# Optimization experiments

Hardware: AMD Instinct MI355X
Metric: run time of the kernel (lower is better)

The kernel has to match this reference:

```python
import jax, jax.numpy as jnp
import numpy as np

B, L, D, H, DFF, MODES, ELAYERS = 64, 512, 512, 8, 2048, 32, 2
VOCAB, NUM_APP, KERNEL = 10000, 10000, 25
E = D // H


def setup_inputs() -> dict:
    key = jax.random.key(0)
    ks = jax.random.split(key, 16)
    scale = 1.0 / (D * D)  # FourierBlock weight init scale
    return {
        'x_app': jax.random.randint(ks[0], (B, L), 0, VOCAB),
        'x_time': jax.random.uniform(ks[1], (B, L), dtype=jnp.float32),
        'time_vecs': jax.random.normal(ks[2], (B, L, 24), dtype=jnp.float32),
        'targets': jax.random.randint(ks[3], (B,), 0, NUM_APP),
        'app_emb_w': jax.random.normal(ks[4], (VOCAB, D), dtype=jnp.float32) * 0.02,
        'time_w': jax.random.normal(ks[5], (D,), dtype=jnp.float32) * 0.02,
        'time_b': jnp.zeros((D,), jnp.float32),
        'Wq': jax.random.normal(ks[6], (ELAYERS, D, D), dtype=jnp.float32) * 0.02,
        'bq': jnp.zeros((ELAYERS, D), jnp.float32),
        'Wo': jax.random.normal(ks[7], (ELAYERS, D, D), dtype=jnp.float32) * 0.02,
        'bo': jnp.zeros((ELAYERS, D), jnp.float32),
        'four_wr': jax.random.uniform(ks[8], (ELAYERS, H, E, E, MODES), dtype=jnp.float32) * scale,
        'four_wi': jax.random.uniform(ks[9], (ELAYERS, H, E, E, MODES), dtype=jnp.float32) * scale,
        'conv1_w': jax.random.normal(ks[10], (ELAYERS, DFF, D), dtype=jnp.float32) * 0.02,
        'conv2_w': jax.random.normal(ks[11], (ELAYERS, D, DFF), dtype=jnp.float32) * 0.02,
        'norm_w': jnp.ones((D,), jnp.float32),
        'norm_b': jnp.zeros((D,), jnp.float32),
        'proj_w': jax.random.normal(ks[12], (NUM_APP, D + 24), dtype=jnp.float32) * 0.02,
        'proj_b': jnp.zeros((NUM_APP,), jnp.float32),
    }


def moving_avg(x):
    # edge-replicate pad by (K-1)//2 on each side, then AvgPool1d(K, stride=1)
    pad = (KERNEL - 1) // 2
    xp = jnp.pad(x, ((0, 0), (pad, pad), (0, 0)), mode='edge')  # [B, L+K-1, D]
    cs = jnp.cumsum(xp, axis=1)
    cs = jnp.concatenate([jnp.zeros_like(cs[:, :1]), cs], axis=1)
    return (cs[:, KERNEL:] - cs[:, :-KERNEL]) / KERNEL  # [B, L, D]


def series_decomp(x):
    m = moving_avg(x)
    return x - m, m


def my_layernorm(x, w, b, eps=1e-5):
    mu = jnp.mean(x, axis=-1, keepdims=True)
    var = jnp.mean((x - mu) ** 2, axis=-1, keepdims=True)
    xh = (x - mu) * jax.lax.rsqrt(var + eps) * w + b
    # my_Layernorm: subtract per-sample mean over the sequence dim
    return xh - jnp.mean(xh, axis=1, keepdims=True)


def fourier_block(q, wr, wi):
    # q: [B, L, H, E] -> [B, H, E, L]
    Bq, Lq, Hq, Eq = q.shape
    x = jnp.transpose(q, (0, 2, 3, 1))
    x_ft = jnp.fft.rfft(x, axis=-1)             # [B,H,E,L//2+1] complex64
    xs = x_ft[..., :MODES]                      # low-frequency mode selection
    w = (wr + 1j * wi).astype(xs.dtype)         # [H,E,E,M]
    out_sel = jnp.einsum('bhim,hiom->bhom', xs, w)
    out_ft = jnp.zeros((Bq, Hq, Eq, Lq // 2 + 1), dtype=xs.dtype).at[..., :MODES].set(out_sel)
    return jnp.fft.irfft(out_ft, n=Lq, axis=-1)  # [B,H,E,L]


def encoder_layer(x, Wq, bq, Wo, bo, wr, wi, c1, c2):
    Bx, Lx, Dx = x.shape
    q = (x @ Wq.T + bq).reshape(Bx, Lx, H, E)
    out = fourier_block(q, wr, wi)               # [B,H,E,L]
    # faithful to torch: out.view(B, L, -1) is a raw row-major reinterpret
    out = out.reshape(Bx, Lx, H * E)
    new_x = out @ Wo.T + bo
    x = x + new_x
    x, _ = series_decomp(x)
    y = jax.nn.relu(jnp.einsum('bld,fd->blf', x, c1))   # conv1 (1x1, no bias)
    y = jnp.einsum('blf,df->bld', y, c2)                # conv2 (1x1, no bias)
    res, _ = series_decomp(x + y)
    return res


def reference(x_app, x_time, time_vecs, targets, app_emb_w, time_w, time_b,
              Wq, bq, Wo, bo, four_wr, four_wi, conv1_w, conv2_w,
              norm_w, norm_b, proj_w, proj_b):
    x = app_emb_w[x_app] + x_time[..., None] * time_w + time_b  # [B,L,D]
    for l in range(ELAYERS):
        x = encoder_layer(x, Wq[l], bq[l], Wo[l], bo[l],
                          four_wr[l], four_wi[l], conv1_w[l], conv2_w[l])
    x = my_layernorm(x, norm_w, norm_b)
    last = x[:, -1, :]                                   # [B,D]
    out = jnp.concatenate([last, time_vecs[:, -1, :]], axis=1)  # [B,D+24]
    score = out @ proj_w.T + proj_b                      # [B,NUM_APP]
    return score  # mode='predict' returns score
```

## Files before the change

### kernel.cpp

```cpp
#include <hip/hip_runtime.h>


typedef unsigned short u16;
typedef float f32x4 __attribute__((ext_vector_type(4)));
typedef __bf16 bf16x8 __attribute__((ext_vector_type(8)));

__device__ __forceinline__ u16 f2b(float f) {
  unsigned u = __float_as_uint(f);
  return (u16)((u + 0x7FFFu + ((u >> 16) & 1u)) >> 16);
}
__device__ __forceinline__ float b2f(u16 v) {
  return __uint_as_float((unsigned)v << 16);
}
__device__ __forceinline__ f32x4 b4f(ushort4 v) {
  f32x4 r;
  r.x = b2f(v.x); r.y = b2f(v.y); r.z = b2f(v.z); r.w = b2f(v.w);
  return r;
}

__device__ __forceinline__ void gll16(const void* g, void* l) {
  __builtin_amdgcn_global_load_lds(
      (const __attribute__((address_space(1))) void*)g,
      (__attribute__((address_space(3))) void*)l, 16, 0, 0);
}

template<bool SWAP>
__device__ __forceinline__ f32x4 mfma16(bf16x8 a, bf16x8 b, f32x4 c) {
  if constexpr (SWAP)
    return __builtin_amdgcn_mfma_f32_16x16x32_bf16(b, a, c, 0, 0, 0);
  else
    return __builtin_amdgcn_mfma_f32_16x16x32_bf16(a, b, c, 0, 0, 0);
}

template<bool BIAS, bool RELU, bool RES, bool OUTBF16, bool GUARD, bool TRANS,
         bool SWZ>
__global__ __launch_bounds__(256, 3)
void k_gemm(const u16* __restrict__ A, const u16* __restrict__ B,
            const float* __restrict__ bias, const u16* __restrict__ res,
            float* __restrict__ Cf, u16* __restrict__ Cb,
            int M, int N, int K,
            long zA, long zB, long zC, int nbn, int nbm)
{
  __shared__ __align__(16) u16 sA[2][128 * 32];
  __shared__ __align__(16) u16 sB[2][128 * 32];
  const int tid = threadIdx.x;
  const int wave = tid >> 6, lane = tid & 63;
  int bn, bm;
  if (SWZ) {
    int bid = blockIdx.x;
    int xcd = bid & 7, loc = bid >> 3;
    bn = loc % nbn;
    bm = xcd * (nbm >> 3) + loc / nbn;
  } else {
    bn = blockIdx.x;
    bm = blockIdx.y;
  }
  const int bz = blockIdx.z;
  const int wm = (wave >> 1) * 64, wn = (wave & 1) * 64;

  A += (size_t)bz * zA;
  B += (size_t)bz * zB;

  const int r0 = tid >> 2;
  const int lg = tid & 3;
  const int ps = lg ^ ((r0 >> 1) & 3);
  int gmA0 = bm * 128 + r0, gmA1 = gmA0 + 64;
  int gnB0 = bn * 128 + r0, gnB1 = gnB0 + 64;
  if (GUARD) {
    gmA0 = gmA0 < M ? gmA0 : M - 1;
    gmA1 = gmA1 < M ? gmA1 : M - 1;
    gnB0 = gnB0 < N ? gnB0 : N - 1;
    gnB1 = gnB1 < N ? gnB1 : N - 1;
  }
  const size_t rb = (size_t)K * 2;
  const char* pa0 = (const char*)A + (size_t)gmA0 * rb + lg * 16;
  const char* pa1 = (const char*)A + (size_t)gmA1 * rb + lg * 16;
  const char* pb0 = (const char*)B + (size_t)gnB0 * rb + lg * 16;
  const char* pb1 = (const char*)B + (size_t)gnB1 * rb + lg * 16;
  const int w0 = r0 * 32 + ps * 8;

  f32x4 acc[4][4];
  const f32x4 z = {0.f, 0.f, 0.f, 0.f};
#pragma unroll
  for (int i = 0; i < 4; ++i)
#pragma unroll
    for (int j = 0; j < 4; ++j) acc[i][j] = z;

  const int r = lane & 15, qd = lane >> 4;
  const int pA = (qd ^ ((lane >> 1) & 3)) * 8;
  const int nk = K >> 5;

  uint4 va0, va1, vb0, vb1;
  auto gload = [&](int kt) {
    const size_t ko = (size_t)kt * 64;
    va0 = *(const uint4*)(pa0 + ko);
    va1 = *(const uint4*)(pa1 + ko);
    vb0 = *(const uint4*)(pb0 + ko);
    vb1 = *(const uint4*)(pb1 + ko);
  };

  gload(0);
  int pg = 0;
  for (int kt = 0; kt < nk; ++kt) {
    *(uint4*)&sA[pg][w0]        = va0;
    *(uint4*)&sA[pg][w0 + 2048] = va1;
    *(uint4*)&sB[pg][w0]        = vb0;
    *(uint4*)&sB[pg][w0 + 2048] = vb1;
    if (kt + 1 < nk) gload(kt + 1);
    __syncthreads();
    bf16x8 af[4], bg[4];
#pragma unroll
    for (int mi = 0; mi < 4; ++mi)
      af[mi] = *(const bf16x8*)&sA[pg][(wm + mi * 16 + r) * 32 + pA];
#pragma unroll
    for (int ni = 0; ni < 4; ++ni)
      bg[ni] = *(const bf16x8*)&sB[pg][(wn + ni * 16 + r) * 32 + pA];
#pragma unroll
    for (int mi = 0; mi < 4; ++mi)
#pragma unroll
      for (int ni = 0; ni < 4; ++ni)
        acc[mi][ni] = mfma16<!TRANS>(af[mi], bg[ni], acc[mi][ni]);
    pg ^= 1;
  }

  if (Cf) Cf += (size_t)bz * zC;
  if (Cb) Cb += (size_t)bz * zC;

  if constexpr (!TRANS) {
#pragma unroll
    for (int mi = 0; mi < 4; ++mi) {
      const int gm = bm * 128 + wm + mi * 16 + r;
      if (GUARD && gm >= M) continue;
#pragma unroll
      for (int ni = 0; ni < 4; ++ni) {
        const int gn0 = bn * 128 + wn + ni * 16 + qd * 4;
        if (GUARD && gn0 >= N) continue;
        float v[4];
        ushort4 rv;
        if (RES) rv = *(const ushort4*)&res[(size_t)gm * N + gn0];
#pragma unroll
        for (int e = 0; e < 4; ++e) {
          v[e] = acc[mi][ni][e];
          if (BIAS) v[e] += bias[gn0 + e];
          if (RES)  v[e] += b2f(e == 0 ? rv.x : e == 1 ? rv.y : e == 2 ? rv.z : rv.w);
          if (RELU) v[e] = v[e] > 0.f ? v[e] : 0.f;
        }
        if (OUTBF16) {
          ushort4 o;
          o.x = f2b(v[0]); o.y = f2b(v[1]); o.z = f2b(v[2]); o.w = f2b(v[3]);
          *(ushort4*)&Cb[(size_t)gm * N + gn0] = o;
        } else {
          float4 o = {v[0], v[1], v[2], v[3]};
          *(float4*)&Cf[(size_t)gm * N + gn0] = o;
        }
      }
    }
  } else {
#pragma unroll
    for (int ni = 0; ni < 4; ++ni) {
      const int gn = bn * 128 + wn + ni * 16 + r;
      if (GUARD && gn >= N) continue;
      const float bb = BIAS ? bias[gn] : 0.f;
#pragma unroll
      for (int mi = 0; mi < 4; ++mi) {
        const int gm0 = bm * 128 + wm + mi * 16 + qd * 4;
        if (GUARD && gm0 >= M) continue;
        float v[4];
#pragma unroll
        for (int e = 0; e < 4; ++e) {
          v[e] = acc[mi][ni][e];
          if (BIAS) v[e] += bb;
          if (RELU) v[e] = v[e] > 0.f ? v[e] : 0.f;
        }
        if (OUTBF16) {
          ushort4 o;
          o.x = f2b(v[0]); o.y = f2b(v[1]); o.z = f2b(v[2]); o.w = f2b(v[3]);
          *(ushort4*)&Cb[(size_t)gn * M + gm0] = o;
        } else {
          float4 o = {v[0], v[1], v[2], v[3]};
          *(float4*)&Cf[(size_t)gn * M + gm0] = o;
        }
      }
    }
  }
}

template<bool BIAS, bool RELU, bool RES, bool TRANS>
__global__ __launch_bounds__(512, 2)
void k_gemm3(const u16* __restrict__ A, const u16* __restrict__ B,
             const float* __restrict__ bias, const u16* __restrict__ res,
             u16* __restrict__ C, int M, int N, int K,
             int nbn, int nbm, long zA, long zC)
{
  __shared__ __align__(16) u16 sA[2][2][256 * 32];
  __shared__ __align__(16) u16 sB[2][2][256 * 32];
  const int tid = threadIdx.x;
  const int w8 = tid >> 6, lane = tid & 63;
  const int bid = blockIdx.x;
  const int xcd = bid & 7, loc = bid >> 3;
  const int mpx = (int)(gridDim.x >> 3) / nbn;
  const int mflat = xcd * mpx + loc / nbn;
  const int bn = loc % nbn;
  const int bz = mflat / nbm;
  const int bm = mflat - bz * nbm;
  const int wm = (w8 >> 2) * 128, wn = (w8 & 3) * 64;

  A += (size_t)bz * zA;

  const int r0 = tid >> 2;
  const int lg = (tid & 3) ^ ((r0 >> 1) & 3);
  const u16* pA0 = A + (size_t)(bm * 256 + r0) * K + lg * 8;
  const u16* pA1 = pA0 + (size_t)128 * K;
  const u16* pB0 = B + (size_t)(bn * 256 + r0) * K + lg * 8;
  const u16* pB1 = pB0 + (size_t)128 * K;
  const int la0 = w8 * 512;
  const int la1 = 4096 + w8 * 512;

  const int nk = K >> 6;

  auto stA = [&](int t, int ks) {
    const size_t ko = (size_t)(t << 6) + (size_t)(ks << 5);
    u16* d = &sA[t & 1][ks][0];
    gll16(pA0 + ko, d + la0);
    gll16(pA1 + ko, d + la1);
  };
  auto stB = [&](int t, int ks) {
    const size_t ko = (size_t)(t << 6) + (size_t)(ks << 5);
    u16* d = &sB[t & 1][ks][0];
    gll16(pB0 + ko, d + la0);
    gll16(pB1 + ko, d + la1);
  };

  f32x4 acc[8][4];
  const f32x4 z = {0.f, 0.f, 0.f, 0.f};
#pragma unroll
  for (int i = 0; i < 8; ++i)
#pragma unroll
    for (int j = 0; j < 4; ++j) acc[i][j] = z;

  const int fr = lane & 15, qd = lane >> 4;
  const int pAo = ((qd ^ ((lane >> 1) & 3)) << 3);

  stA(0, 0); stB(0, 0); stA(0, 1); stB(0, 1);
  if (nk > 1) { stA(1, 0); stB(1, 0); }
  asm volatile("s_waitcnt vmcnt(8)" ::: "memory");
  __builtin_amdgcn_s_barrier();

  for (int t = 0; t < nk; ++t) {
    const int c = t & 1;
    bf16x8 af[4], bgk[4];
#pragma unroll
    for (int i = 0; i < 4; ++i)
      af[i] = *(const bf16x8*)&sA[c][0][(wm + i * 16 + fr) * 32 + pAo];
#pragma unroll
    for (int i = 0; i < 4; ++i)
      bgk[i] = *(const bf16x8*)&sB[c][0][(wn + i * 16 + fr) * 32 + pAo];
    if (t + 1 < nk) stA(t + 1, 1);
    asm volatile("s_waitcnt vmcnt(8)" ::: "memory");
    __builtin_amdgcn_s_barrier();
    __builtin_amdgcn_s_setprio(1);
#pragma unroll
    for (int mi = 0; mi < 4; ++mi)
#pragma unroll
      for (int ni = 0; ni < 4; ++ni)
        acc[mi][ni] = __builtin_amdgcn_mfma_f32_16x16x32_bf16(
            af[mi], bgk[ni], acc[mi][ni], 0, 0, 0);
    __builtin_amdgcn_s_setprio(0);
    __builtin_amdgcn_s_barrier();
#pragma unroll
    for (int i = 0; i < 4; ++i)
      af[i] = *(const bf16x8*)&sA[c][0][(wm + 64 + i * 16 + fr) * 32 + pAo];
    if (t + 1 < nk) stB(t + 1, 1);
    if (t == nk - 1) asm volatile("s_waitcnt vmcnt(0)" ::: "memory");
    else             asm volatile("s_waitcnt vmcnt(8)" ::: "memory");
    __builtin_amdgcn_s_barrier();
    __builtin_amdgcn_s_setprio(1);
#pragma unroll
    for (int mi = 0; mi < 4; ++mi)
#pragma unroll
      for (int ni = 0; ni < 4; ++ni)
        acc[4 + mi][ni] = __builtin_amdgcn_mfma_f32_16x16x32_bf16(
            af[mi], bgk[ni], acc[4 + mi][ni], 0, 0, 0);
    __builtin_amdgcn_s_setprio(0);
    __builtin_amdgcn_s_barrier();
#pragma unroll
    for (int i = 0; i < 4; ++i)
      af[i] = *(const bf16x8*)&sA[c][1][(wm + i * 16 + fr) * 32 + pAo];
#pragma unroll
    for (int i = 0; i < 4; ++i)
      bgk[i] = *(const bf16x8*)&sB[c][1][(wn + i * 16 + fr) * 32 + pAo];
    if (t + 2 < nk) stA(t + 2, 0);
    asm volatile("s_waitcnt vmcnt(8)" ::: "memory");
    __builtin_amdgcn_s_barrier();
    __builtin_amdgcn_s_setprio(1);
#pragma unroll
    for (int mi = 0; mi < 4; ++mi)
#pragma unroll
      for (int ni = 0; ni < 4; ++ni)
        acc[mi][ni] = __builtin_amdgcn_mfma_f32_16x16x32_bf16(
            af[mi], bgk[ni], acc[mi][ni], 0, 0, 0);
    __builtin_amdgcn_s_setprio(0);
    __builtin_amdgcn_s_barrier();
#pragma unroll
    for (int i = 0; i < 4; ++i)
      af[i] = *(const bf16x8*)&sA[c][1][(wm + 64 + i * 16 + fr) * 32 + pAo];
    if (t + 2 < nk) stB(t + 2, 0);
    if (t == nk - 2) asm volatile("s_waitcnt vmcnt(4)" ::: "memory");
    else             asm volatile("s_waitcnt vmcnt(8)" ::: "memory");
    __builtin_amdgcn_s_barrier();
    __builtin_amdgcn_s_setprio(1);
#pragma unroll
    for (int mi = 0; mi < 4; ++mi)
#pragma unroll
      for (int ni = 0; ni < 4; ++ni)
        acc[4 + mi][ni] = __builtin_amdgcn_mfma_f32_16x16x32_bf16(
            af[mi], bgk[ni], acc[4 + mi][ni], 0, 0, 0);
    __builtin_amdgcn_s_setprio(0);
    __builtin_amdgcn_s_barrier();
  }

  C += (size_t)bz * zC;
#pragma unroll
  for (int mi = 0; mi < 8; ++mi) {
#pragma unroll
    for (int ni = 0; ni < 4; ++ni) {
#pragma unroll
      for (int e = 0; e < 4; ++e) {
        int gm = bm * 256 + wm + mi * 16 + qd * 4 + e;
        int gn = bn * 256 + wn + ni * 16 + fr;
        float v = acc[mi][ni][e];
        if (BIAS) v += bias[gn];
        if (RES)  v += b2f(res[(size_t)gm * N + gn]);
        if (RELU) v = v > 0.f ? v : 0.f;
        size_t oi = TRANS ? ((size_t)gn * M + gm) : ((size_t)gm * N + gn);
        C[oi] = f2b(v);
      }
    }
  }
}

__global__ void k_basis(u16* __restrict__ dftB, u16* __restrict__ Binv)
{
  int id = blockIdx.x * 256 + threadIdx.x;
  if (id >= 32768) return;
  {
    int m = id >> 9, l = id & 511;
    int mm = m & 31;
    float ang = (float)((l * mm) & 511) * (6.283185307179586f / 512.f);
    float s, c;
    __sincosf(ang, &s, &c);
    dftB[id] = f2b(m < 32 ? c : -s);
  }
  {
    int l = id >> 6, m = id & 63;
    int mm = m & 31;
    float ang = (float)((l * mm) & 511) * (6.283185307179586f / 512.f);
    float s, c;
    __sincosf(ang, &s, &c);
    float v;
    if (m < 32) v = (m == 0 ? 1.f : 2.f) * (1.f / 512.f) * c;
    else        v = (mm == 0 ? 0.f : (-2.f / 512.f) * s);
    Binv[id] = f2b(v);
  }
}

__global__ void k_convert4(const float* __restrict__ wq, u16* __restrict__ wqo,
                           const float* __restrict__ wo, u16* __restrict__ woo,
                           const float* __restrict__ c1, u16* __restrict__ c1o,
                           const float* __restrict__ c2, u16* __restrict__ c2o)
{
  int id = blockIdx.x * 256 + threadIdx.x;
  if (id < 524288)       wqo[id]           = f2b(wq[id]);
  else if (id < 1048576) woo[id - 524288]  = f2b(wo[id - 524288]);
  else if (id < 3145728) c1o[id - 1048576] = f2b(c1[id - 1048576]);
  else                   c2o[id - 3145728] = f2b(c2[id - 3145728]);
}

__global__ void k_convproj(const float* __restrict__ w, u16* __restrict__ o)
{
  int id = blockIdx.x * 256 + threadIdx.x;
  if (id >= 10000 * 544) return;
  int n = id / 544, k = id % 544;
  o[id] = f2b(k < 536 ? w[(size_t)n * 536 + k] : 0.f);
}

__global__ void k_transp(const float* __restrict__ wr, const float* __restrict__ wi,
                         float* __restrict__ wrT, float* __restrict__ wiT)
{
  __shared__ float tr[64 * 33], ti[64 * 33];
  int blk = blockIdx.x;
  int t = threadIdx.x;
  int lh = blk >> 6, i = blk & 63;
  const size_t src = (size_t)blk * 2048;
#pragma unroll
  for (int p = 0; p < 8; ++p) {
    int id = p * 256 + t;
    int o = id >> 5, m = id & 31;
    tr[o * 33 + m] = wr[src + id];
    ti[o * 33 + m] = wi[src + id];
  }
  __syncthreads();
#pragma unroll
  for (int p = 0; p < 8; ++p) {
    int id = p * 256 + t;
    int m = id >> 6, o = id & 63;
    size_t dst = ((size_t)(lh * 32 + m) * 64 + i) * 64 + o;
    wrT[dst] = tr[o * 33 + m];
    wiT[dst] = ti[o * 33 + m];
  }
}

__global__ void k_embed(const int* __restrict__ xapp, const float* __restrict__ xtime,
                        const float* __restrict__ emb, const float* __restrict__ tw,
                        const float* __restrict__ tb, u16* __restrict__ xb)
{
  int id = blockIdx.x * 256 + threadIdx.x;
  int j = id & 127, bl = id >> 7;
  float4 e = ((const float4*)emb)[(size_t)xapp[bl] * 128 + j];
  float t = xtime[bl];
  float4 w4 = ((const float4*)tw)[j];
  float4 b4 = ((const float4*)tb)[j];
  ushort4 o;
  o.x = f2b(e.x + t * w4.x + b4.x);
  o.y = f2b(e.y + t * w4.y + b4.y);
  o.z = f2b(e.z + t * w4.z + b4.z);
  o.w = f2b(e.w + t * w4.w + b4.w);
  ((ushort4*)xb)[id] = o;
}

__global__ __launch_bounds__(256)
void k_mix(const float* __restrict__ spec, const float* __restrict__ wrT,
           const float* __restrict__ wiT, u16* __restrict__ Ab)
{
  __shared__ float swr[4096], swi[4096];
  __shared__ float sre[4][64], sim[4][64];
  int hm = blockIdx.x;
  int bg = blockIdx.y;
  int h = hm >> 5, m = hm & 31, t = threadIdx.x;
  const float* wrb = wrT + (size_t)hm * 4096;
  const float* wib = wiT + (size_t)hm * 4096;
#pragma unroll
  for (int p = 0; p < 16; ++p) {
    int id = p * 256 + t;
    swr[id] = wrb[id];
    swi[id] = wib[id];
  }
  int o = t & 63, bsub = t >> 6;
  for (int b0 = 0; b0 < 16; b0 += 4) {
    __syncthreads();
    int b = bg * 16 + b0 + bsub;
    const float* spb = spec + (size_t)b * 32768;
    sre[bsub][o] = spb[m * 512 + h * 64 + o];
    sim[bsub][o] = spb[(32 + m) * 512 + h * 64 + o];
    __syncthreads();
    float aR = 0.f, aI = 0.f;
#pragma unroll 8
    for (int i = 0; i < 64; ++i) {
      float xr = sre[bsub][i], xi = sim[bsub][i];
      float wrv = swr[i * 64 + o], wiv = swi[i * 64 + o];
      aR += xr * wrv - xi * wiv;
      aI += xr * wiv + xi * wrv;
    }
    size_t row = (size_t)b * 512 + h * 64 + o;
    Ab[row * 64 + m] = f2b(aR);
    Ab[row * 64 + 32 + m] = f2b(aI);
  }
}

__global__ void k_decomp(const u16* __restrict__ in, u16* __restrict__ outb)
{
  int blk = blockIdx.x;
  int j = blk >> 3;
  int b = (blk & 7) + 8 * (j >> 3);
  int ck = (j & 7) * 2 + (threadIdx.x >> 7);
  int d4 = threadIdx.x & 127;
  const ushort4* xb = (const ushort4*)(in + (size_t)b * 262144) + d4;
  ushort4* ob = (ushort4*)(outb + (size_t)b * 262144) + d4;
  int l0 = ck * 32;
  f32x4 sum = {0.f, 0.f, 0.f, 0.f};
#pragma unroll
  for (int jj = -12; jj <= 12; ++jj) {
    int idx = l0 + jj;
    idx = idx < 0 ? 0 : idx;
    sum += b4f(xb[idx * 128]);
  }
#pragma unroll 4
  for (int l = l0; l < l0 + 32; ++l) {
    f32x4 xv = b4f(xb[l * 128]);
    f32x4 o = xv - sum * (1.f / 25.f);
    ushort4 ov;
    ov.x = f2b(o.x); ov.y = f2b(o.y); ov.z = f2b(o.z); ov.w = f2b(o.w);
    ob[l * 128] = ov;
    int ia = l + 13 > 511 ? 511 : l + 13;
    int ir = l - 12 < 0 ? 0 : l - 12;
    sum += b4f(xb[ia * 128]) - b4f(xb[ir * 128]);
  }
}

__global__ void k_lnstats(const u16* __restrict__ x, float* __restrict__ mu,
                          float* __restrict__ rs)
{
  int row = blockIdx.x;
  const u16* xr = x + (size_t)row * 512;
  int t = threadIdx.x;
  ushort2 p = ((const ushort2*)xr)[t];
  float v0 = b2f(p.x), v1 = b2f(p.y);
  float s = v0 + v1, ss = v0 * v0 + v1 * v1;
#pragma unroll
  for (int off = 32; off; off >>= 1) {
    s += __shfl_down(s, off);
    ss += __shfl_down(ss, off);
  }
  __shared__ float as[4], ass[4];
  if ((t & 63) == 0) { as[t >> 6] = s; ass[t >> 6] = ss; }
  __syncthreads();
  if (t == 0) {
    float S = as[0] + as[1] + as[2] + as[3];
    float SS = ass[0] + ass[1] + ass[2] + ass[3];
    float m = S * (1.f / 512.f);
    float var = SS * (1.f / 512.f) - m * m;
    mu[row] = m;
    rs[row] = rsqrtf(var + 1e-5f);
  }
}

__global__ void k_lastcat1(const u16* __restrict__ x, const float* __restrict__ mu,
                           const float* __restrict__ rs, float* __restrict__ part)
{
  int b = blockIdx.x >> 3, g = blockIdx.x & 7, t = threadIdx.x;
  const u16* xb = x + (size_t)b * 262144;
  const float* mub = mu + b * 512;
  const float* rsb = rs + b * 512;
  float a0 = 0.f, a1 = 0.f;
#pragma unroll 4
  for (int l = g * 64; l < g * 64 + 64; ++l) {
    float m = mub[l], rr = rsb[l];
    ushort2 p = ((const ushort2*)(xb + l * 512))[t];
    a0 += (b2f(p.x) - m) * rr;
    a1 += (b2f(p.y) - m) * rr;
  }
  part[((size_t)b * 8 + g) * 512 + 2 * t]     = a0;
  part[((size_t)b * 8 + g) * 512 + 2 * t + 1] = a1;
}

__global__ void k_lastcat2(const u16* __restrict__ x, const float* __restrict__ mu,
                           const float* __restrict__ rs, const float* __restrict__ part,
                           const float* __restrict__ nw, u16* __restrict__ cat)
{
  int b = blockIdx.x, t = threadIdx.x;
#pragma unroll
  for (int hh = 0; hh < 2; ++hh) {
    int d = t + hh * 256;
    float acc = 0.f;
#pragma unroll
    for (int g = 0; g < 8; ++g)
      acc += part[((size_t)b * 8 + g) * 512 + d];
    float lastv = (b2f(x[(size_t)b * 262144 + 511 * 512 + d]) - mu[b * 512 + 511])
                  * rs[b * 512 + 511];
    cat[b * 544 + d] = f2b(nw[d] * (lastv - acc * (1.f / 512.f)));
  }
}

__global__ void k_timecat(const float* __restrict__ tv, u16* __restrict__ cat)
{
  int id = blockIdx.x * 256 + threadIdx.x;
  if (id >= 2048) return;
  int b = id >> 5, j = id & 31;
  int pos = 512 + j;
  float v = (pos < 536) ? tv[((size_t)b * 512 + 511) * 24 + (pos - 512)] : 0.f;
  cat[b * 544 + pos] = f2b(v);
}

extern "C" void kernel_launch(void* const* d_in, const int* in_sizes, int n_in,
                              void* d_out, int out_size, void* d_ws, size_t ws_size,
                              hipStream_t stream)
{
  (void)in_sizes; (void)n_in; (void)out_size; (void)ws_size;
  const int*   x_app  = (const int*)  d_in[0];
  const float* x_time = (const float*)d_in[1];
  const float* tvec   = (const float*)d_in[2];
  const float* emb    = (const float*)d_in[4];
  const float* time_w = (const float*)d_in[5];
  const float* time_b = (const float*)d_in[6];
  const float* Wq     = (const float*)d_in[7];
  const float* bq     = (const float*)d_in[8];
  const float* Wo     = (const float*)d_in[9];
  const float* bo     = (const float*)d_in[10];
  const float* fwr    = (const float*)d_in[11];
  const float* fwi    = (const float*)d_in[12];
  const float* c1     = (const float*)d_in[13];
  const float* c2     = (const float*)d_in[14];
  const float* norm_w = (const float*)d_in[15];
  const float* proj_w = (const float*)d_in[17];
  const float* proj_b = (const float*)d_in[18];
  float* out = (float*)d_out;

  char* w = (char*)d_ws;
  auto alloc = [&](size_t bytes) -> char* {
    char* p = w;
    w += (bytes + 255) & ~(size_t)255;
    return p;
  };
  u16*   Cb   = (u16*)  alloc(33554432);
  u16*   YqT  = (u16*)  alloc(134217728);
  u16*   T1b  = (u16*)  alloc(33554432);
  float* S1   = (float*)alloc(8388608);
  u16*   Coef = (u16*)  alloc(4194304);
  float* wrT  = (float*)alloc(2 * 1048576 * 4);
  float* wiT  = (float*)alloc(2 * 1048576 * 4);
  u16*   wqb  = (u16*)  alloc(2 * 262144 * 2);
  u16*   wob  = (u16*)  alloc(2 * 262144 * 2);
  u16*   c1b  = (u16*)  alloc(2 * 1048576 * 2);
  u16*   c2b  = (u16*)  alloc(2 * 1048576 * 2);
  u16*   pwb  = (u16*)  alloc(10000 * 544 * 2);
  u16*   dftB = (u16*)  alloc(64 * 512 * 2);
  u16*   Binv = (u16*)  alloc(512 * 64 * 2);
  float* muB  = (float*)alloc(131072);
  float* rsB  = (float*)alloc(131072);
  float* part = (float*)alloc(64 * 8 * 512 * 4);
  u16*   cat  = (u16*)  alloc(64 * 544 * 2);

  k_basis<<<128, 256, 0, stream>>>(dftB, Binv);
  k_transp<<<1024, 256, 0, stream>>>(fwr, fwi, wrT, wiT);
  k_convert4<<<20480, 256, 0, stream>>>(Wq, wqb, Wo, wob, c1, c1b, c2, c2b);
  k_convproj<<<21250, 256, 0, stream>>>(proj_w, pwb);
  k_embed<<<16384, 256, 0, stream>>>(x_app, x_time, emb, time_w, time_b, Cb);

  for (int l = 0; l < 2; ++l) {
    const u16* wq_l = wqb + l * 262144;
    const u16* wo_l = wob + l * 262144;
    const u16* c1_l = c1b + l * 1048576;
    const u16* c2_l = c2b + l * 1048576;

    k_gemm3<true, false, false, true>
        <<<256, 512, 0, stream>>>(
        Cb, wq_l, bq + l * 512, nullptr, YqT, 512, 512, 512,
        2, 2, 262144, 262144);
    k_gemm<false, false, false, false, true, true, false>
        <<<dim3(1, 4, 64), 256, 0, stream>>>(
        YqT, dftB, nullptr, nullptr, S1, nullptr, 512, 64, 512,
        262144, 0, 32768, 0, 0);
    k_mix<<<dim3(256, 4), 256, 0, stream>>>(
        S1, wrT + l * 1048576, wiT + l * 1048576, Coef);
    k_gemm<false, false, false, true, false, false, true>
        <<<dim3(1024, 1, 1), 256, 0, stream>>>(
        Coef, Binv, nullptr, nullptr, nullptr, YqT, 32768, 512, 64,
        0, 0, 0, 4, 256);
    k_gemm3<true, false, true, false>
        <<<256, 512, 0, stream>>>(
        YqT, wo_l, bo + l * 512, Cb, T1b, 32768, 512, 512,
        2, 128, 0, 0);
    k_decomp<<<512, 256, 0, stream>>>(T1b, Cb);
    k_gemm3<false, true, false, false>
        <<<1024, 512, 0, stream>>>(
        Cb, c1_l, nullptr, nullptr, YqT, 32768, 2048, 512,
        8, 128, 0, 0);
    k_gemm3<false, false, true, false>
        <<<256, 512, 0, stream>>>(
        YqT, c2_l, nullptr, Cb, T1b, 32768, 512, 2048,
        2, 128, 0, 0);
    k_decomp<<<512, 256, 0, stream>>>(T1b, Cb);
  }

  k_lnstats<<<32768, 256, 0, stream>>>(Cb, muB, rsB);
  k_lastcat1<<<512, 256, 0, stream>>>(Cb, muB, rsB, part);
  k_lastcat2<<<64, 256, 0, stream>>>(Cb, muB, rsB, part, norm_w, cat);
  k_timecat<<<8, 256, 0, stream>>>(tvec, cat);
  k_gemm<true, false, false, false, true, false, false>
      <<<dim3(79, 1, 1), 256, 0, stream>>>(
      cat, pwb, proj_b, nullptr, out, nullptr, 64, 10000, 544,
      0, 0, 0, 0, 0);
}
```

Before: 835.7 us.

## Fold output projection Wo into inverse DFT basis to drop one GEMM

Precomputes a combined matrix Wo·Binv (512x64 per layer) so the inverse-DFT GEMM directly produces the Wo projection plus bias and residual. This removes the separate 32768x512x512 GEMM and the intermediate YqT write/read per layer, replacing it with a K=64 GEMM. The fold relies on the raw reshape mapping channels consistently, and the folded weights are rounded to bf16 once, which changes rounding slightly.

```diff
diff --git a/kernel.cpp b/kernel.cpp
--- a/kernel.cpp
+++ b/kernel.cpp
@@ -364,16 +364,34 @@
   }
 }
 
-__global__ void k_convert4(const float* __restrict__ wq, u16* __restrict__ wqo,
-                           const float* __restrict__ wo, u16* __restrict__ woo,
+__global__ void k_wb(const float* __restrict__ wo, const u16* __restrict__ Binv,
+                     u16* __restrict__ wb)
+{
+  __shared__ float part[4][64];
+  int blk = blockIdx.x;
+  int t = threadIdx.x;
+  int m = t & 63, q = t >> 6;
+  const float* wrow = wo + (size_t)blk * 512;
+  float a = 0.f;
+#pragma unroll 4
+  for (int l = q * 128; l < q * 128 + 128; ++l)
+    a += wrow[l] * b2f(Binv[l * 64 + m]);
+  part[q][m] = a;
+  __syncthreads();
+  if (t < 64) {
+    float v = part[0][t] + part[1][t] + part[2][t] + part[3][t];
+    wb[(size_t)blk * 64 + t] = f2b(v);
+  }
+}
+
+__global__ void k_convert3(const float* __restrict__ wq, u16* __restrict__ wqo,
                            const float* __restrict__ c1, u16* __restrict__ c1o,
                            const float* __restrict__ c2, u16* __restrict__ c2o)
 {
   int id = blockIdx.x * 256 + threadIdx.x;
   if (id < 524288)       wqo[id]           = f2b(wq[id]);
-  else if (id < 1048576) woo[id - 524288]  = f2b(wo[id - 524288]);
-  else if (id < 3145728) c1o[id - 1048576] = f2b(c1[id - 1048576]);
-  else                   c2o[id - 3145728] = f2b(c2[id - 3145728]);
+  else if (id < 2621440) c1o[id - 524288]  = f2b(c1[id - 524288]);
+  else                   c2o[id - 2621440] = f2b(c2[id - 2621440]);
 }
 
 __global__ void k_convproj(const float* __restrict__ w, u16* __restrict__ o)
@@ -609,7 +627,7 @@
   float* wrT  = (float*)alloc(2 * 1048576 * 4);
   float* wiT  = (float*)alloc(2 * 1048576 * 4);
   u16*   wqb  = (u16*)  alloc(2 * 262144 * 2);
-  u16*   wob  = (u16*)  alloc(2 * 262144 * 2);
+  u16*   wbb  = (u16*)  alloc(2 * 512 * 64 * 2);
   u16*   c1b  = (u16*)  alloc(2 * 1048576 * 2);
   u16*   c2b  = (u16*)  alloc(2 * 1048576 * 2);
   u16*   pwb  = (u16*)  alloc(10000 * 544 * 2);
@@ -621,14 +639,15 @@
   u16*   cat  = (u16*)  alloc(64 * 544 * 2);
 
   k_basis<<<128, 256, 0, stream>>>(dftB, Binv);
+  k_wb<<<1024, 256, 0, stream>>>(Wo, Binv, wbb);
   k_transp<<<1024, 256, 0, stream>>>(fwr, fwi, wrT, wiT);
-  k_convert4<<<20480, 256, 0, stream>>>(Wq, wqb, Wo, wob, c1, c1b, c2, c2b);
+  k_convert3<<<18432, 256, 0, stream>>>(Wq, wqb, c1, c1b, c2, c2b);
   k_convproj<<<21250, 256, 0, stream>>>(proj_w, pwb);
   k_embed<<<16384, 256, 0, stream>>>(x_app, x_time, emb, time_w, time_b, Cb);
 
   for (int l = 0; l < 2; ++l) {
     const u16* wq_l = wqb + l * 262144;
-    const u16* wo_l = wob + l * 262144;
+    const u16* wb_l = wbb + l * 32768;
     const u16* c1_l = c1b + l * 1048576;
     const u16* c2_l = c2b + l * 1048576;
 
@@ -642,14 +661,10 @@
         262144, 0, 32768, 0, 0);
     k_mix<<<dim3(256, 4), 256, 0, stream>>>(
         S1, wrT + l * 1048576, wiT + l * 1048576, Coef);
-    k_gemm<false, false, false, true, false, false, true>
+    k_gemm<true, false, true, true, false, false, true>
         <<<dim3(1024, 1, 1), 256, 0, stream>>>(
-        Coef, Binv, nullptr, nullptr, nullptr, YqT, 32768, 512, 64,
+        Coef, wb_l, bo + l * 512, Cb, nullptr, T1b, 32768, 512, 64,
         0, 0, 0, 4, 256);
-    k_gemm3<true, false, true, false>
-        <<<256, 512, 0, stream>>>(
-        YqT, wo_l, bo + l * 512, Cb, T1b, 32768, 512, 512,
-        2, 128, 0, 0);
     k_decomp<<<512, 256, 0, stream>>>(T1b, Cb);
     k_gemm3<false, true, false, false>
         <<<1024, 512, 0, stream>>>(
```

After: 805.4 us. 3.6% less time.
